# Performance work log

Measured on AMD Instinct MI355X. Metric: run time of the kernel, lower is better.

## Reference

```python
import jax, jax.numpy as jnp
import numpy as np

B, D, N = 2, 64, 512          # batch, channel dim, flattened spatial tokens
H = 4 * D                     # hidden_dim default = input_dim * 4
OUT = D                       # output_dim default = input_dim


def setup_inputs() -> dict:
    key = jax.random.key(0)
    ks = jax.random.split(key, 11)
    s = 0.02
    inp = {
        "input": jax.random.normal(ks[0], (B, D, N), dtype=jnp.float32),
        # inner MLP: Linear(2D->H), ReLU, Linear(H->H), ReLU, Linear(H->H)
        "w1": jax.random.normal(ks[1], (2 * D, H), dtype=jnp.float32) * s,
        "b1": jnp.zeros((H,), jnp.float32),
        "w2": jax.random.normal(ks[2], (H, H), dtype=jnp.float32) * s,
        "b2": jnp.zeros((H,), jnp.float32),
        "w3": jax.random.normal(ks[3], (H, H), dtype=jnp.float32) * s,
        "b3": jnp.zeros((H,), jnp.float32),
        # outer MLP: Linear(H->H), ReLU, Linear(H->OUT)
        "w4": jax.random.normal(ks[4], (H, H), dtype=jnp.float32) * s,
        "b4": jnp.zeros((H,), jnp.float32),
        "w5": jax.random.normal(ks[5], (H, OUT), dtype=jnp.float32) * s,
        "b5": jnp.zeros((OUT,), jnp.float32),
    }
    return inp


def reference(input, w1, b1, w2, b2, w3, b3, w4, b4, w5, b5):
    # channels-first -> channels-last, flatten spatial: [B, N, D]
    x = jnp.transpose(input, (0, 2, 1))
    d = x.shape[-1]
    # pairs[b, c, i] = concat(x[b, i], x[b, c]); decompose first linear:
    # pairs @ w1 = x_i @ w1[:D] + x_c @ w1[D:], avoiding the [B,N,N,2D] cat tensor.
    hi = x @ w1[:d]   # input part, indexed by dim 2 -> [B, N, H]
    hc = x @ w1[d:]   # context part, indexed by dim 1 -> [B, N, H]
    h = jax.nn.relu(hi[:, None, :, :] + hc[:, :, None, :] + b1)  # [B, N, N, H]
    h = jax.nn.relu(h @ w2 + b2)
    h = h @ w3 + b3
    mid = h.sum(axis=(1, 2))              # sum(1).sum(1) -> [B, H]; mid nonlinearity = Identity
    o = jax.nn.relu(mid @ w4 + b4)
    return o @ w5 + b5                     # [B, OUT]
```

## Files before the change

kernel.cpp:

```cpp
#include <hip/hip_runtime.h>


using f32x16  = __attribute__((ext_vector_type(16))) float;
using short8  = __attribute__((ext_vector_type(8))) short;
using float4v = __attribute__((ext_vector_type(4))) float;

__device__ __forceinline__ short f2bf(float f) {
    unsigned u = __float_as_uint(f);
    unsigned r = u + 0x7FFFu + ((u >> 16) & 1u);
    return (short)(r >> 16);
}

__device__ __forceinline__ short8 relu_pack8(float4v lo, float4v hi4) {
#pragma unroll
    for (int e = 0; e < 4; ++e) {
        lo[e]  = fmaxf(lo[e], 0.f);
        hi4[e] = fmaxf(hi4[e], 0.f);
    }
    union { short8 s; unsigned u[4]; } r;
    asm("v_cvt_pk_bf16_f32 %0, %1, %2" : "=v"(r.u[0]) : "v"(lo[0]),  "v"(lo[1]));
    asm("v_cvt_pk_bf16_f32 %0, %1, %2" : "=v"(r.u[1]) : "v"(lo[2]),  "v"(lo[3]));
    asm("v_cvt_pk_bf16_f32 %0, %1, %2" : "=v"(r.u[2]) : "v"(hi4[0]), "v"(hi4[1]));
    asm("v_cvt_pk_bf16_f32 %0, %1, %2" : "=v"(r.u[3]) : "v"(hi4[2]), "v"(hi4[3]));
    return r.s;
}

__global__ __launch_bounds__(256) void prep(const float* __restrict__ in,
                                            const float* __restrict__ w1,
                                            const float* __restrict__ b1,
                                            const float* __restrict__ w2,
                                            float* __restrict__ hi,
                                            float* __restrict__ hcb,
                                            short* __restrict__ bfrag) {
    int tid = threadIdx.x;
    int bidx = blockIdx.x;
    if (bidx < 256) {
        int b = bidx >> 7, n0 = (bidx & 127) * 4;
        __shared__ float xs[4][64];
        {
            int nn = tid >> 6, d = tid & 63;
            xs[nn][d] = in[(size_t)(b * 64 + d) * 512 + n0 + nn];
        }
        __syncthreads();
        float a0[4] = {0.f, 0.f, 0.f, 0.f}, a1[4] = {0.f, 0.f, 0.f, 0.f};
#pragma unroll 8
        for (int d = 0; d < 64; ++d) {
            float wA = w1[d * 256 + tid];
            float wB = w1[(64 + d) * 256 + tid];
#pragma unroll
            for (int nn = 0; nn < 4; ++nn) {
                a0[nn] += xs[nn][d] * wA;
                a1[nn] += xs[nn][d] * wB;
            }
        }
        float bb = b1[tid];
#pragma unroll
        for (int nn = 0; nn < 4; ++nn) {
            size_t o = (size_t)(b * 512 + n0 + nn) * 256 + tid;
            hi[o]  = a0[nn];
            hcb[o] = a1[nn] + bb;
        }
    } else {
        int idx = (bidx - 256) * 256 + tid;
        int k = idx >> 8, ncol = idx & 255;
        int n = ncol >> 5, col = ncol & 31;
        int kk = k >> 4, h = (k >> 3) & 1, j = k & 7;
        int off = (((n * 16 + kk) * 64) + h * 32 + col) * 8 + j;
        bfrag[off] = f2bf(w2[k * 256 + ncol]);
    }
}

__global__ __launch_bounds__(512, 1) void big(const float* __restrict__ hi_,
                                              const float* __restrict__ hcb_,
                                              const short8* __restrict__ bfrag,
                                              const float* __restrict__ b2,
                                              float* __restrict__ partials) {
    __shared__ __align__(16) short8 Blds[8192];
    __shared__ __align__(16) float hcLds[8 * 260];

    const int tid = threadIdx.x;
    const int bid = blockIdx.x;
    const int b = bid >> 7, r = bid & 127;
    const int C = r >> 1;

#pragma unroll
    for (int q = 0; q < 16; ++q) Blds[q * 512 + tid] = bfrag[q * 512 + tid];
    {
        int row = tid >> 6, j4 = (tid & 63) * 4;
        float4v v = *reinterpret_cast<const float4v*>(
            hcb_ + (size_t)b * 131072 + (size_t)(C * 8 + row) * 256 + j4);
        *reinterpret_cast<float4v*>(&hcLds[row * 260 + j4]) = v;
    }
    __syncthreads();

    const int w = tid >> 6, lane = tid & 63;
    const int l31 = lane & 31, h = lane >> 5;
    const int ip = l31 & 7, cq4 = l31 >> 3;

    const int Ibase = (r & 1) * 32 + w * 4;

    const float* __restrict__ hib = hi_ + (size_t)b * 131072;
    const float* __restrict__ hcl0 = &hcLds[cq4 * 260 + h * 8];
    const float* __restrict__ hcl1 = &hcLds[(cq4 + 4) * 260 + h * 8];

    float b2v[8];
#pragma unroll
    for (int n = 0; n < 8; ++n) b2v[n] = b2[n * 32 + l31];
    float jobsum[8] = {0.f, 0.f, 0.f, 0.f, 0.f, 0.f, 0.f, 0.f};

#pragma unroll 1
    for (int t = 0; t < 4; ++t) {
        const int I = Ibase + t;
        const float* __restrict__ hirow = hib + (size_t)(I * 8 + ip) * 256 + h * 8;

        short8 A0[16], A1[16];
#pragma unroll
        for (int kk = 0; kk < 16; ++kk) {
            float4v x0  = *reinterpret_cast<const float4v*>(hirow + kk * 16);
            float4v x1  = *reinterpret_cast<const float4v*>(hirow + kk * 16 + 4);
            float4v c00 = *reinterpret_cast<const float4v*>(hcl0 + kk * 16);
            float4v c01 = *reinterpret_cast<const float4v*>(hcl0 + kk * 16 + 4);
            float4v c10 = *reinterpret_cast<const float4v*>(hcl1 + kk * 16);
            float4v c11 = *reinterpret_cast<const float4v*>(hcl1 + kk * 16 + 4);
            A0[kk] = relu_pack8(x0 + c00, x1 + c01);
            A1[kk] = relu_pack8(x0 + c10, x1 + c11);
            if (kk & 1) __builtin_amdgcn_sched_barrier(0);
        }

#pragma unroll 1
        for (int np = 0; np < 4; ++np) {
            f32x16 aA0, aB0, aA1, aB1;
#pragma unroll
            for (int e = 0; e < 16; ++e) {
                aA0[e] = b2v[np];     aB0[e] = b2v[np];
                aA1[e] = b2v[np + 4]; aB1[e] = b2v[np + 4];
            }
            const short8* __restrict__ bl0 = Blds + np * 1024 + lane;
            const short8* __restrict__ bl1 = Blds + (np + 4) * 1024 + lane;
            __builtin_amdgcn_s_setprio(1);
#pragma unroll
            for (int kk = 0; kk < 16; ++kk) {
                short8 bf0 = bl0[kk * 64];
                short8 bf1 = bl1[kk * 64];
                aA0 = __builtin_amdgcn_mfma_f32_32x32x16_bf16(A0[kk], bf0, aA0, 0, 0, 0);
                aB0 = __builtin_amdgcn_mfma_f32_32x32x16_bf16(A1[kk], bf0, aB0, 0, 0, 0);
                aA1 = __builtin_amdgcn_mfma_f32_32x32x16_bf16(A0[kk], bf1, aA1, 0, 0, 0);
                aB1 = __builtin_amdgcn_mfma_f32_32x32x16_bf16(A1[kk], bf1, aB1, 0, 0, 0);
            }
            __builtin_amdgcn_s_setprio(0);
            float s0 = 0.f, s1 = 0.f;
#pragma unroll
            for (int e = 0; e < 16; ++e) {
                s0 += fmaxf(aA0[e], 0.f) + fmaxf(aB0[e], 0.f);
                s1 += fmaxf(aA1[e], 0.f) + fmaxf(aB1[e], 0.f);
            }
            jobsum[np]     += s0;
            jobsum[np + 4] += s1;
        }
    }

#pragma unroll
    for (int n = 0; n < 8; ++n) {
        jobsum[n] += __shfl_xor(jobsum[n], 32);
        if (h == 0)
            partials[((size_t)(b * 256 + n * 32 + l31)) * 1024 + r * 8 + w] = jobsum[n];
    }
}

__global__ __launch_bounds__(256) void reduceK(const float* __restrict__ partials,
                                               float* __restrict__ su_g) {
    int tid = threadIdx.x, blk = blockIdx.x;
    const float4v* pv = reinterpret_cast<const float4v*>(partials + (size_t)blk * 1024);
    float4v v = pv[tid];
    float s = v[0] + v[1] + v[2] + v[3];
#pragma unroll
    for (int d = 1; d < 64; d <<= 1) s += __shfl_xor(s, d);
    __shared__ float wsum[4];
    if ((tid & 63) == 0) wsum[tid >> 6] = s;
    __syncthreads();
    if (tid == 0) su_g[blk] = wsum[0] + wsum[1] + wsum[2] + wsum[3];
}

__global__ __launch_bounds__(512) void finalK(const float* __restrict__ su_g,
                                              const float* __restrict__ w3,
                                              const float* __restrict__ b3,
                                              const float* __restrict__ w4,
                                              const float* __restrict__ b4,
                                              const float* __restrict__ w5,
                                              const float* __restrict__ b5,
                                              float* __restrict__ out) {
    __shared__ float su[2][256], mid[2][256], o[2][256];
    int tid = threadIdx.x;
    int b = tid >> 8, c = tid & 255;
    su[b][c] = su_g[b * 256 + c];
    __syncthreads();
    float m = 262144.0f * b3[c];
    for (int k = 0; k < 256; ++k) m += su[b][k] * w3[k * 256 + c];
    mid[b][c] = m;
    __syncthreads();
    float ov = b4[c];
    for (int k = 0; k < 256; ++k) ov += mid[b][k] * w4[k * 256 + c];
    o[b][c] = fmaxf(ov, 0.f);
    __syncthreads();
    if (c < 64) {
        float rr = b5[c];
        for (int k = 0; k < 256; ++k) rr += o[b][k] * w5[k * 64 + c];
        out[b * 64 + c] = rr;
    }
}

extern "C" void kernel_launch(void* const* d_in, const int* in_sizes, int n_in,
                              void* d_out, int out_size, void* d_ws, size_t ws_size,
                              hipStream_t stream) {
    const float* in = (const float*)d_in[0];
    const float* w1 = (const float*)d_in[1];
    const float* b1 = (const float*)d_in[2];
    const float* w2 = (const float*)d_in[3];
    const float* b2 = (const float*)d_in[4];
    const float* w3 = (const float*)d_in[5];
    const float* b3 = (const float*)d_in[6];
    const float* w4 = (const float*)d_in[7];
    const float* b4 = (const float*)d_in[8];
    const float* w5 = (const float*)d_in[9];
    const float* b5 = (const float*)d_in[10];
    float* out = (float*)d_out;

    char* ws = (char*)d_ws;
    float* hi       = (float*)(ws);
    float* hcb      = (float*)(ws + (1u << 20));
    short* bfrag    = (short*)(ws + (2u << 20));
    float* partials = (float*)(ws + (2u << 20) + (1u << 18));
    float* su_g     = (float*)(ws + (4u << 20) + (1u << 18));

    prep<<<512, 256, 0, stream>>>(in, w1, b1, w2, hi, hcb, bfrag);
    big<<<256, 512, 0, stream>>>(hi, hcb, (const short8*)bfrag, b2, partials);
    reduceK<<<512, 256, 0, stream>>>(partials, su_g);
    finalK<<<1, 512, 0, stream>>>(su_g, w3, b3, w4, b4, w5, b5, out);
}
```

Measured before the change: 89.73 us.

## Double waves per block and give each wave a single A tile

The big kernel now runs 1024 threads per block, and each wave builds and multiplies only one 32-row A fragment set instead of two. The context rows are read straight from global memory, no longer staged in LDS. The work split moves from block halves to one block per 4-column group, and the partials buffer and reduction are doubled to match. The aim is more waves to hide latency with fewer registers per wave. The cost is losing the reuse of each B fragment across two MFMAs, more LDS reads per MFMA, and a launch-bounds hint that may force heavy register limits or spills.

```diff
diff --git a/kernel.cpp b/kernel.cpp
--- a/kernel.cpp
+++ b/kernel.cpp
@@ -70,38 +70,28 @@
     }
 }
 
-__global__ __launch_bounds__(512, 1) void big(const float* __restrict__ hi_,
-                                              const float* __restrict__ hcb_,
-                                              const short8* __restrict__ bfrag,
-                                              const float* __restrict__ b2,
-                                              float* __restrict__ partials) {
+__global__ __launch_bounds__(1024, 4) void big(const float* __restrict__ hi_,
+                                               const float* __restrict__ hcb_,
+                                               const short8* __restrict__ bfrag,
+                                               const float* __restrict__ b2,
+                                               float* __restrict__ partials) {
     __shared__ __align__(16) short8 Blds[8192];
-    __shared__ __align__(16) float hcLds[8 * 260];
 
     const int tid = threadIdx.x;
     const int bid = blockIdx.x;
-    const int b = bid >> 7, r = bid & 127;
-    const int C = r >> 1;
-
-#pragma unroll
-    for (int q = 0; q < 16; ++q) Blds[q * 512 + tid] = bfrag[q * 512 + tid];
-    {
-        int row = tid >> 6, j4 = (tid & 63) * 4;
-        float4v v = *reinterpret_cast<const float4v*>(
-            hcb_ + (size_t)b * 131072 + (size_t)(C * 8 + row) * 256 + j4);
-        *reinterpret_cast<float4v*>(&hcLds[row * 260 + j4]) = v;
-    }
+    const int b = bid >> 7, cq = bid & 127;
+
+#pragma unroll
+    for (int q = 0; q < 8; ++q) Blds[q * 1024 + tid] = bfrag[q * 1024 + tid];
     __syncthreads();
 
     const int w = tid >> 6, lane = tid & 63;
     const int l31 = lane & 31, h = lane >> 5;
     const int ip = l31 & 7, cq4 = l31 >> 3;
 
-    const int Ibase = (r & 1) * 32 + w * 4;
-
     const float* __restrict__ hib = hi_ + (size_t)b * 131072;
-    const float* __restrict__ hcl0 = &hcLds[cq4 * 260 + h * 8];
-    const float* __restrict__ hcl1 = &hcLds[(cq4 + 4) * 260 + h * 8];
+    const float* __restrict__ hcl = hcb_ + (size_t)b * 131072
+                                  + (size_t)(cq * 4 + cq4) * 256 + h * 8;
 
     float b2v[8];
 #pragma unroll
@@ -110,52 +100,42 @@
 
 #pragma unroll 1
     for (int t = 0; t < 4; ++t) {
-        const int I = Ibase + t;
+        const int I = w * 4 + t;
         const float* __restrict__ hirow = hib + (size_t)(I * 8 + ip) * 256 + h * 8;
 
-        short8 A0[16], A1[16];
+        short8 A[16];
 #pragma unroll
         for (int kk = 0; kk < 16; ++kk) {
-            float4v x0  = *reinterpret_cast<const float4v*>(hirow + kk * 16);
-            float4v x1  = *reinterpret_cast<const float4v*>(hirow + kk * 16 + 4);
-            float4v c00 = *reinterpret_cast<const float4v*>(hcl0 + kk * 16);
-            float4v c01 = *reinterpret_cast<const float4v*>(hcl0 + kk * 16 + 4);
-            float4v c10 = *reinterpret_cast<const float4v*>(hcl1 + kk * 16);
-            float4v c11 = *reinterpret_cast<const float4v*>(hcl1 + kk * 16 + 4);
-            A0[kk] = relu_pack8(x0 + c00, x1 + c01);
-            A1[kk] = relu_pack8(x0 + c10, x1 + c11);
-            if (kk & 1) __builtin_amdgcn_sched_barrier(0);
+            float4v x0 = *reinterpret_cast<const float4v*>(hirow + kk * 16);
+            float4v x1 = *reinterpret_cast<const float4v*>(hirow + kk * 16 + 4);
+            float4v c0 = *reinterpret_cast<const float4v*>(hcl + kk * 16);
+            float4v c1 = *reinterpret_cast<const float4v*>(hcl + kk * 16 + 4);
+            A[kk] = relu_pack8(x0 + c0, x1 + c1);
+            if ((kk & 3) == 3) __builtin_amdgcn_sched_barrier(0);
         }
 
 #pragma unroll 1
-        for (int np = 0; np < 4; ++np) {
-            f32x16 aA0, aB0, aA1, aB1;
-#pragma unroll
-            for (int e = 0; e < 16; ++e) {
-                aA0[e] = b2v[np];     aB0[e] = b2v[np];
-                aA1[e] = b2v[np + 4]; aB1[e] = b2v[np + 4];
-            }
-            const short8* __restrict__ bl0 = Blds + np * 1024 + lane;
-            const short8* __restrict__ bl1 = Blds + (np + 4) * 1024 + lane;
+        for (int n = 0; n < 8; ++n) {
+            f32x16 acc;
+#pragma unroll
+            for (int e = 0; e < 16; ++e) acc = (e == 0) ? acc : acc;
+#pragma unroll
+            for (int e = 0; e < 16; ++e) acc[e] = b2v[n];
+            const short8* __restrict__ bl = Blds + n * 1024 + lane;
             __builtin_amdgcn_s_setprio(1);
 #pragma unroll
             for (int kk = 0; kk < 16; ++kk) {
-                short8 bf0 = bl0[kk * 64];
-                short8 bf1 = bl1[kk * 64];
-                aA0 = __builtin_amdgcn_mfma_f32_32x32x16_bf16(A0[kk], bf0, aA0, 0, 0, 0);
-                aB0 = __builtin_amdgcn_mfma_f32_32x32x16_bf16(A1[kk], bf0, aB0, 0, 0, 0);
-                aA1 = __builtin_amdgcn_mfma_f32_32x32x16_bf16(A0[kk], bf1, aA1, 0, 0, 0);
-                aB1 = __builtin_amdgcn_mfma_f32_32x32x16_bf16(A1[kk], bf1, aB1, 0, 0, 0);
+                short8 bf = bl[kk * 64];
+                acc = __builtin_amdgcn_mfma_f32_32x32x16_bf16(A[kk], bf, acc, 0, 0, 0);
             }
             __builtin_amdgcn_s_setprio(0);
             float s0 = 0.f, s1 = 0.f;
 #pragma unroll
-            for (int e = 0; e < 16; ++e) {
-                s0 += fmaxf(aA0[e], 0.f) + fmaxf(aB0[e], 0.f);
-                s1 += fmaxf(aA1[e], 0.f) + fmaxf(aB1[e], 0.f);
+            for (int e = 0; e < 16; e += 2) {
+                s0 += fmaxf(acc[e], 0.f);
+                s1 += fmaxf(acc[e + 1], 0.f);
             }
-            jobsum[np]     += s0;
-            jobsum[np + 4] += s1;
+            jobsum[n] += s0 + s1;
         }
     }
 
@@ -163,16 +143,17 @@
     for (int n = 0; n < 8; ++n) {
         jobsum[n] += __shfl_xor(jobsum[n], 32);
         if (h == 0)
-            partials[((size_t)(b * 256 + n * 32 + l31)) * 1024 + r * 8 + w] = jobsum[n];
+            partials[((size_t)(b * 256 + n * 32 + l31)) * 2048 + cq * 16 + w] = jobsum[n];
     }
 }
 
 __global__ __launch_bounds__(256) void reduceK(const float* __restrict__ partials,
                                                float* __restrict__ su_g) {
     int tid = threadIdx.x, blk = blockIdx.x;
-    const float4v* pv = reinterpret_cast<const float4v*>(partials + (size_t)blk * 1024);
-    float4v v = pv[tid];
-    float s = v[0] + v[1] + v[2] + v[3];
+    const float4v* pv = reinterpret_cast<const float4v*>(partials + (size_t)blk * 2048);
+    float4v v0 = pv[tid];
+    float4v v1 = pv[tid + 256];
+    float s = v0[0] + v0[1] + v0[2] + v0[3] + v1[0] + v1[1] + v1[2] + v1[3];
 #pragma unroll
     for (int d = 1; d < 64; d <<= 1) s += __shfl_xor(s, d);
     __shared__ float wsum[4];
@@ -230,10 +211,10 @@
     float* hcb      = (float*)(ws + (1u << 20));
     short* bfrag    = (short*)(ws + (2u << 20));
     float* partials = (float*)(ws + (2u << 20) + (1u << 18));
-    float* su_g     = (float*)(ws + (4u << 20) + (1u << 18));
+    float* su_g     = (float*)(ws + (6u << 20) + (1u << 18));
 
     prep<<<512, 256, 0, stream>>>(in, w1, b1, w2, hi, hcb, bfrag);
-    big<<<256, 512, 0, stream>>>(hi, hcb, (const short8*)bfrag, b2, partials);
+    big<<<256, 1024, 0, stream>>>(hi, hcb, (const short8*)bfrag, b2, partials);
     reduceK<<<512, 256, 0, stream>>>(partials, su_g);
     finalK<<<1, 512, 0, stream>>>(su_g, w3, b3, w4, b4, w5, b5, out);
 }
```

Measured after the change: 113.9 us. 27.0% more time.
